# Kernel optimization log

Measured on AMD Instinct MI355X. Metric: run time of the kernel, lower is better.

## Reference

```python
import jax, jax.numpy as jnp
import numpy as np

BS, S, D_IN, D_EMB = 256, 256, 512, 1024
RATIO = 0.3
BN_EPS = 1e-5
VOCAB = 49408


def setup_inputs() -> dict:
    key = jax.random.key(0)
    ks = jax.random.split(key, 12)
    features = jax.random.normal(ks[0], (BS, S, D_IN), dtype=jnp.float32)
    # variable-length token sequences: nonzero ids up to length, 0-padded
    lengths = jax.random.randint(ks[1], (BS,), 3, S + 1)
    tok = jax.random.randint(ks[2], (BS, S), 1, VOCAB)
    text = jnp.where(jnp.arange(S)[None, :] < lengths[:, None], tok, 0).astype(jnp.int32)
    atten = jax.random.normal(ks[3], (BS, S, S), dtype=jnp.float32)
    sc = 0.02
    H = D_EMB // 2  # 512, MLP hidden
    params = {
        "lin_w": jax.random.normal(ks[4], (D_IN, D_EMB), dtype=jnp.float32) * sc,
        "lin_b": jnp.zeros((D_EMB,), dtype=jnp.float32),
        "w1": jax.random.normal(ks[5], (D_IN, H), dtype=jnp.float32) * sc,
        "b1": jnp.zeros((H,), dtype=jnp.float32),
        "g1": jnp.ones((H,), dtype=jnp.float32),
        "be1": jnp.zeros((H,), dtype=jnp.float32),
        "w2": jax.random.normal(ks[6], (H, D_EMB), dtype=jnp.float32) * sc,
        "b2": jnp.zeros((D_EMB,), dtype=jnp.float32),
        "g2": jnp.ones((D_EMB,), dtype=jnp.float32),
        "be2": jnp.zeros((D_EMB,), dtype=jnp.float32),
    }
    return {"features": features, "text": text, "atten": atten, **params}


def _bn_train(x, g, b):
    # BatchNorm1d in train mode: biased batch stats over rows
    m = x.mean(axis=0)
    v = x.var(axis=0)
    return (x - m) * jax.lax.rsqrt(v + BN_EPS) * g + b


def reference(features, text, atten, lin_w, lin_b, w1, b1, g1, be1, w2, b2, g2, be2):
    bs, seq_len = atten.shape[0], atten.shape[1]
    mask = (text != 0).astype(jnp.float32)          # (bs, S)
    token_lens = mask.sum(axis=1)                   # (bs,)
    k = max(1, int((seq_len - 2) * RATIO))          # static
    eos_pos = jnp.clip(token_lens - 1, 0, seq_len - 1).astype(jnp.int32)
    bidx = jnp.arange(bs)
    # scatter writes into atten (faithful to torch in-place updates)
    atten = atten.at[:, :, 0].set(-1.0)
    atten = atten.at[bidx, :, eos_pos].set(-1.0)
    atten = atten.at[bidx, eos_pos, :].set(-1.0)
    atten_sel = atten[bidx, eos_pos, :] * mask      # (bs, S)
    _, topk_idx = jax.lax.top_k(atten_sel, k)       # (bs, k)
    feats_k = jnp.take_along_axis(features, topk_idx[:, :, None], axis=1)  # (bs,k,D_in)
    norm = jnp.maximum(jnp.linalg.norm(feats_k, axis=-1, keepdims=True), 1e-6)
    feats_k = feats_k / norm
    # linear branch
    cap_emb = jnp.einsum("bkd,de->bke", feats_k, lin_w) + lin_b
    # MLP branch: Linear -> BN -> ReLU -> Linear (last layer no BN/ReLU)
    x = feats_k.reshape(bs * k, -1)
    h = jax.nn.relu(_bn_train(x @ w1 + b1, g1, be1))
    o = (h @ w2 + b2).reshape(bs, k, -1)
    fused = o + cap_emb                             # (bs,k,D_emb)
    # maxk_pool1d_var with k=1: max over first pool_lens[i] positions
    pool_lens = jnp.clip(token_lens - 2, 1, k).astype(jnp.int32)
    valid = jnp.arange(k)[None, :] < pool_lens[:, None]  # (bs,k)
    out = jnp.max(jnp.where(valid[:, :, None], fused, -jnp.inf), axis=1)
    return out.astype(jnp.float32)
```

## Files before the change

### kernel.cpp

```cpp
#include <hip/hip_runtime.h>
#include <hip/hip_bf16.h>

typedef __bf16 bf16;
typedef __bf16 bf16x4 __attribute__((ext_vector_type(4)));
typedef __bf16 bf16x8 __attribute__((ext_vector_type(8)));
typedef float  f32x4  __attribute__((ext_vector_type(4)));

#define BSZ   256
#define SEQ   256
#define DIN   512
#define DEMB  1024
#define KSEL  76
#define MROWS (BSZ * KSEL)
#define MT256 (MROWS / 256)
#define PART76 (MT256 * 512)
#define NRED  19

__device__ __forceinline__ void gload16(const void* g, void* l) {
  __builtin_amdgcn_global_load_lds((const __attribute__((address_space(1))) void*)g,
                                   (__attribute__((address_space(3))) void*)l, 16, 0, 0);
}

__device__ __forceinline__ unsigned enc(float v) {
  unsigned u = __float_as_uint(v);
  return (u & 0x80000000u) ? ~u : (u | 0x80000000u);
}
__device__ __forceinline__ float dec(unsigned k) {
  return (k & 0x80000000u) ? __uint_as_float(k ^ 0x80000000u) : __uint_as_float(~k);
}

__global__ void k_setup(const int* __restrict__ text, int* __restrict__ topk,
                        int* __restrict__ plen, uint4* __restrict__ keys4,
                        const float* __restrict__ w1, bf16* __restrict__ w1t,
                        const float* __restrict__ lin_w, const float* __restrict__ w2,
                        bf16* __restrict__ b2t,
                        const float* __restrict__ lin_b, const float* __restrict__ b2,
                        float* __restrict__ bias2) {
  int blk = blockIdx.x, tid = threadIdx.x;
  if (blk < 256) {
    int b = blk;
    keys4[b * 256 + tid] = make_uint4(0u, 0u, 0u, 0u);
    __shared__ int red[256];
    red[tid] = (text[b * SEQ + tid] != 0) ? 1 : 0;
    __syncthreads();
    for (int s = 128; s > 0; s >>= 1) {
      if (tid < s) red[tid] += red[tid + s];
      __syncthreads();
    }
    int len = red[0];
    int z = SEQ - len;
    if (tid < KSEL) topk[b * KSEL + tid] = (tid < z) ? (len + tid) : (tid - z);
    if (tid == 0) {
      int p = len - 2;
      plen[b] = p < 1 ? 1 : (p > KSEL ? KSEL : p);
    }
  } else if (blk < 1536) {
    const float* W;
    bf16* Wt;
    int N, ldo, bx, by;
    if (blk < 512)       { int t = blk - 256;  W = w1;    Wt = w1t;       N = 512;  ldo = 512;  bx = t & 15; by = t >> 4; }
    else if (blk < 1024) { int t = blk - 512;  W = lin_w; Wt = b2t;       N = 1024; ldo = 1024; bx = t & 31; by = t >> 5; }
    else                 { int t = blk - 1024; W = w2;    Wt = b2t + 512; N = 1024; ldo = 1024; bx = t & 31; by = t >> 5; }
    __shared__ float tile[32][33];
    int tx = tid & 31, ty = tid >> 5;
    int n = bx * 32 + tx, k0 = by * 32;
#pragma unroll
    for (int r = 0; r < 32; r += 8)
      tile[ty + r][tx] = W[(size_t)(k0 + ty + r) * N + n];
    __syncthreads();
#pragma unroll
    for (int r = 0; r < 32; r += 8)
      Wt[(size_t)(bx * 32 + ty + r) * ldo + k0 + tx] = (bf16)tile[tx][ty + r];
  } else {
    int i = (blk - 1536) * 256 + tid;
    bias2[i] = lin_b[i] + b2[i];
  }
}

__global__ void k_gather(const float* __restrict__ feats, const int* __restrict__ topk,
                         bf16* __restrict__ A2) {
  int r = blockIdx.x;
  int b = r / KSEL;
  int src = topk[r];
  const float4* row = (const float4*)(feats + ((size_t)b * SEQ + src) * DIN);
  int t = threadIdx.x;
  float4 v = row[t];
  float ss = v.x * v.x + v.y * v.y + v.z * v.z + v.w * v.w;
#pragma unroll
  for (int o = 32; o > 0; o >>= 1) ss += __shfl_down(ss, o);
  __shared__ float wsum[2];
  if ((t & 63) == 0) wsum[t >> 6] = ss;
  __syncthreads();
  float total = wsum[0] + wsum[1];
  float inv = 1.0f / fmaxf(sqrtf(total), 1e-6f);
  bf16x4 o4;
  o4.x = (bf16)(v.x * inv);
  o4.y = (bf16)(v.y * inv);
  o4.z = (bf16)(v.z * inv);
  o4.w = (bf16)(v.w * inv);
  ((bf16x4*)A2)[(size_t)r * 256 + t] = o4;
}

template<int EPI>
__global__ __launch_bounds__(512, 2)
void k_gemm(const bf16* __restrict__ A, int lda, const bf16* __restrict__ Bt, int ldb,
            const float* __restrict__ bias, bf16* __restrict__ Cb, int ldc, int Kext,
            int nbx, float* __restrict__ part, const int* __restrict__ plen,
            unsigned* __restrict__ keys) {
  __shared__ __align__(16) bf16 As[3][256 * 64];
  __shared__ __align__(16) bf16 Bs[3][128 * 64];
  const int q = gridDim.x >> 3;
  const int lid = blockIdx.x;
  const int wg = (lid & 7) * q + (lid >> 3);
  const int bx = wg % nbx, by = wg / nbx;
  const int m0 = by * 256, n0 = bx * 128;
  const int tid = threadIdx.x, wid = tid >> 6, lane = tid & 63;
  const int wm = wid >> 1, wn = wid & 1;
  const int srow = lane >> 3;
  const int scol = ((lane & 7) ^ srow) * 8;
  const bf16* Ag = A + (size_t)(m0 + wid * 16 + srow) * lda + scol;
  const bf16* Bg = Bt + (size_t)(n0 + wid * 16 + srow) * ldb + scol;
  const int nT = Kext >> 6;
  f32x4 acc[4][4] = {};
  const int fr = lane & 15, fg = lane >> 4;

  auto stageA = [&](int t, int buf) {
    const int kt = t << 6;
#pragma unroll
    for (int c = 0; c < 2; ++c) {
      gload16(Ag + (size_t)(c * 8) * lda + kt, &As[buf][(wid * 16 + c * 8) * 64]);
      gload16(Ag + (size_t)(128 + c * 8) * lda + kt, &As[buf][(128 + wid * 16 + c * 8) * 64]);
    }
  };
  auto stageB = [&](int t, int buf) {
    const int kt = t << 6;
#pragma unroll
    for (int c = 0; c < 2; ++c)
      gload16(Bg + (size_t)(c * 8) * ldb + kt, &Bs[buf][(wid * 16 + c * 8) * 64]);
  };

  stageA(0, 0); stageB(0, 0);
  stageA(1, 1); stageB(1, 1);
  asm volatile("s_waitcnt vmcnt(6)" ::: "memory");
  __builtin_amdgcn_s_barrier();
  __builtin_amdgcn_sched_barrier(0);

  int pb = 0, ps = 2;
  for (int t = 0; t < nT; ++t) {
    bf16x8 a0[4], b0[4], a1[4], b1[4];
#pragma unroll
    for (int i = 0; i < 4; ++i)
      a0[i] = *(const bf16x8*)&As[pb][(wm * 64 + i * 16 + fr) * 64 + (fg ^ (fr & 7)) * 8];
#pragma unroll
    for (int j = 0; j < 4; ++j)
      b0[j] = *(const bf16x8*)&Bs[pb][(wn * 64 + j * 16 + fr) * 64 + (fg ^ (fr & 7)) * 8];
    __builtin_amdgcn_sched_barrier(0);
    if (t + 2 < nT) stageA(t + 2, ps);
#pragma unroll
    for (int i = 0; i < 4; ++i)
      a1[i] = *(const bf16x8*)&As[pb][(wm * 64 + i * 16 + fr) * 64 + ((4 | fg) ^ (fr & 7)) * 8];
#pragma unroll
    for (int j = 0; j < 4; ++j)
      b1[j] = *(const bf16x8*)&Bs[pb][(wn * 64 + j * 16 + fr) * 64 + ((4 | fg) ^ (fr & 7)) * 8];
    if (t + 2 < nT) stageB(t + 2, ps);
    asm volatile("s_waitcnt lgkmcnt(8)" ::: "memory");
    __builtin_amdgcn_sched_barrier(0);
    __builtin_amdgcn_s_setprio(1);
#pragma unroll
    for (int i = 0; i < 4; ++i)
#pragma unroll
      for (int j = 0; j < 4; ++j)
        acc[i][j] = __builtin_amdgcn_mfma_f32_16x16x32_bf16(a0[i], b0[j], acc[i][j], 0, 0, 0);
    __builtin_amdgcn_s_setprio(0);
    asm volatile("s_waitcnt lgkmcnt(0)" ::: "memory");
    __builtin_amdgcn_sched_barrier(0);
    __builtin_amdgcn_s_setprio(1);
#pragma unroll
    for (int i = 0; i < 4; ++i)
#pragma unroll
      for (int j = 0; j < 4; ++j)
        acc[i][j] = __builtin_amdgcn_mfma_f32_16x16x32_bf16(a1[i], b1[j], acc[i][j], 0, 0, 0);
    __builtin_amdgcn_s_setprio(0);
    if (t + 2 < nT) {
      asm volatile("s_waitcnt vmcnt(6)" ::: "memory");
    } else {
      asm volatile("s_waitcnt vmcnt(0)" ::: "memory");
    }
    __builtin_amdgcn_s_barrier();
    __builtin_amdgcn_sched_barrier(0);
    pb = (pb == 2) ? 0 : pb + 1;
    ps = (ps == 2) ? 0 : ps + 1;
  }

  float bv[4];
#pragma unroll
  for (int j = 0; j < 4; ++j) bv[j] = bias[n0 + wn * 64 + j * 16 + fr];

  if (EPI == 1) {
    float s[4] = {0, 0, 0, 0}, qq_[4] = {0, 0, 0, 0};
#pragma unroll
    for (int i = 0; i < 4; ++i)
#pragma unroll
      for (int v = 0; v < 4; ++v) {
        int r = m0 + wm * 64 + i * 16 + fg * 4 + v;
        bf16* crow = Cb + (size_t)r * ldc + n0 + wn * 64 + fr;
#pragma unroll
        for (int j = 0; j < 4; ++j) {
          float val = acc[i][j][v] + bv[j];
          crow[j * 16] = (bf16)val;
          s[j] += val;
          qq_[j] += val * val;
        }
      }
#pragma unroll
    for (int j = 0; j < 4; ++j) {
      s[j] += __shfl_down(s[j], 32); s[j] += __shfl_down(s[j], 16);
      qq_[j] += __shfl_down(qq_[j], 32); qq_[j] += __shfl_down(qq_[j], 16);
    }
    __syncthreads();
    float* red = (float*)&As[0][0];
    if (lane < 16) {
#pragma unroll
      for (int j = 0; j < 4; ++j) {
        red[(wid * 4 + j) * 16 + lane] = s[j];
        red[512 + (wid * 4 + j) * 16 + lane] = qq_[j];
      }
    }
    __syncthreads();
    if (tid < 128) {
      int c = tid;
      int wnsel = c >> 6, jj = (c >> 4) & 3, ff = c & 15;
      float ss = 0, qs = 0;
#pragma unroll
      for (int wmi = 0; wmi < 4; ++wmi) {
        ss += red[((wmi * 2 + wnsel) * 4 + jj) * 16 + ff];
        qs += red[512 + ((wmi * 2 + wnsel) * 4 + jj) * 16 + ff];
      }
      part[by * 512 + n0 + c] = ss;
      part[PART76 + by * 512 + n0 + c] = qs;
    }
  } else {
    const float NEG = -__builtin_huge_valf();
    int cur_b = -1, pl = 0;
    bool any = false;
    float cm[4] = {NEG, NEG, NEG, NEG};
#pragma unroll
    for (int i = 0; i < 4; ++i)
#pragma unroll
      for (int v = 0; v < 4; ++v) {
        int gr = m0 + wm * 64 + i * 16 + fg * 4 + v;
        int b = gr / KSEL;
        if (b != cur_b) {
          if (any) {
#pragma unroll
            for (int j = 0; j < 4; ++j)
              atomicMax(&keys[(size_t)cur_b * DEMB + n0 + wn * 64 + j * 16 + fr], enc(cm[j]));
          }
          cur_b = b;
          pl = plen[b];
          any = false;
#pragma unroll
          for (int j = 0; j < 4; ++j) cm[j] = NEG;
        }
        if (gr - b * KSEL < pl) {
          any = true;
#pragma unroll
          for (int j = 0; j < 4; ++j) cm[j] = fmaxf(cm[j], acc[i][j][v] + bv[j]);
        }
      }
    if (any) {
#pragma unroll
      for (int j = 0; j < 4; ++j)
        atomicMax(&keys[(size_t)cur_b * DEMB + n0 + wn * 64 + j * 16 + fr], enc(cm[j]));
    }
  }
}

__global__ void k_bnredA(const float* __restrict__ part, float* __restrict__ part2) {
  int i = blockIdx.x, t = threadIdx.x;
  float s0 = 0, s1 = 0, q0 = 0, q1 = 0;
  for (int j = 0; j < 4; ++j) {
    const float* p = part + (size_t)(i * 4 + j) * 512 + t * 2;
    float2 v = *(const float2*)p;
    float2 u = *(const float2*)(p + PART76);
    s0 += v.x; s1 += v.y; q0 += u.x; q1 += u.y;
  }
  part2[i * 512 + t * 2] = s0;
  part2[i * 512 + t * 2 + 1] = s1;
  part2[NRED * 512 + i * 512 + t * 2] = q0;
  part2[NRED * 512 + i * 512 + t * 2 + 1] = q1;
}

__global__ void k_bnstats(const float* __restrict__ part2, const float* __restrict__ g1,
                          const float* __restrict__ be1, float* __restrict__ bns) {
  int c = threadIdx.x;
  float s = 0, q = 0;
  for (int i = 0; i < NRED; ++i) {
    s += part2[i * 512 + c];
    q += part2[NRED * 512 + i * 512 + c];
  }
  const float invn = 1.0f / (float)MROWS;
  float mean = s * invn;
  float var = q * invn - mean * mean;
  float sc = rsqrtf(var + 1e-5f) * g1[c];
  bns[c] = sc;
  bns[512 + c] = be1[c] - mean * sc;
}

__global__ void k_bnapply(bf16x8* __restrict__ A2v, const float* __restrict__ bns) {
  size_t idx = (size_t)blockIdx.x * 256 + threadIdx.x;
  size_t row = idx >> 6;
  int c = (int)(idx & 63);
  bf16x8* p = A2v + row * 128 + 64 + c;
  bf16x8 v = *p;
  int c8 = c * 8;
  const float4 s0 = *(const float4*)(bns + c8);
  const float4 s1 = *(const float4*)(bns + c8 + 4);
  const float4 h0 = *(const float4*)(bns + 512 + c8);
  const float4 h1 = *(const float4*)(bns + 512 + c8 + 4);
  bf16x8 o;
  o[0] = (bf16)fmaxf(fmaf((float)v[0], s0.x, h0.x), 0.0f);
  o[1] = (bf16)fmaxf(fmaf((float)v[1], s0.y, h0.y), 0.0f);
  o[2] = (bf16)fmaxf(fmaf((float)v[2], s0.z, h0.z), 0.0f);
  o[3] = (bf16)fmaxf(fmaf((float)v[3], s0.w, h0.w), 0.0f);
  o[4] = (bf16)fmaxf(fmaf((float)v[4], s1.x, h1.x), 0.0f);
  o[5] = (bf16)fmaxf(fmaf((float)v[5], s1.y, h1.y), 0.0f);
  o[6] = (bf16)fmaxf(fmaf((float)v[6], s1.z, h1.z), 0.0f);
  o[7] = (bf16)fmaxf(fmaf((float)v[7], s1.w, h1.w), 0.0f);
  *p = o;
}

__global__ void k_decode(const unsigned* __restrict__ keys, float* __restrict__ out) {
  int i = blockIdx.x * 256 + threadIdx.x;
  out[i] = dec(keys[i]);
}

extern "C" void kernel_launch(void* const* d_in, const int* in_sizes, int n_in,
                              void* d_out, int out_size, void* d_ws, size_t ws_size,
                              hipStream_t stream) {
  const float* features = (const float*)d_in[0];
  const int*   text     = (const int*)d_in[1];
  const float* lin_w    = (const float*)d_in[3];
  const float* lin_b    = (const float*)d_in[4];
  const float* w1       = (const float*)d_in[5];
  const float* b1       = (const float*)d_in[6];
  const float* g1       = (const float*)d_in[7];
  const float* be1      = (const float*)d_in[8];
  const float* w2       = (const float*)d_in[9];
  const float* b2       = (const float*)d_in[10];
  float* out = (float*)d_out;
  char* ws = (char*)d_ws;

  int*      topk  = (int*)(ws + 0);
  int*      plen  = (int*)(ws + 77824);
  float*    bns   = (float*)(ws + 78848);
  float*    bias2 = (float*)(ws + 82944);
  float*    part  = (float*)(ws + 87040);
  float*    part2 = (float*)(ws + 398336);
  bf16*     w1t   = (bf16*)(ws + 476160);
  bf16*     b2t   = (bf16*)(ws + 1000448);
  bf16*     A2    = (bf16*)(ws + 3097600);
  unsigned* keys  = (unsigned*)(ws + 42943488);

  k_setup<<<1540, 256, 0, stream>>>(text, topk, plen, (uint4*)keys,
                                    w1, w1t, lin_w, w2, b2t, lin_b, b2, bias2);
  k_gather<<<MROWS, 128, 0, stream>>>(features, topk, A2);
  k_gemm<1><<<MT256 * 4, 512, 0, stream>>>(A2, 1024, w1t, 512, b1, A2 + 512, 1024,
                                           512, 4, part, nullptr, nullptr);
  k_bnredA<<<NRED, 256, 0, stream>>>(part, part2);
  k_bnstats<<<1, 512, 0, stream>>>(part2, g1, be1, bns);
  k_bnapply<<<4864, 256, 0, stream>>>((bf16x8*)A2, bns);
  k_gemm<2><<<MT256 * 8, 512, 0, stream>>>(A2, 1024, b2t, 1024, bias2, nullptr, 0,
                                           1024, 8, nullptr, plen, keys);
  k_decode<<<BSZ * DEMB / 256, 256, 0, stream>>>(keys, out);
}
```

Measured before the change: 130.7 us.

## Restructure GEMM to 4 waves with 128x64 warp tiles and K=32 stages

The GEMM block drops from 8 waves to 4, and each wave now computes a 128x64 output tile (8x4 MFMA fragments) instead of 64x64. The K step per stage goes from 64 to 32, which halves LDS use per buffer, and the XOR swizzle is changed to match the 32-wide rows. The two-half interleaving of LDS reads with MFMAs is replaced by a single load-wait-compute phase. The goal is more register-level reuse per LDS fragment and higher occupancy from the smaller LDS footprint, at the cost of more accumulator registers, more barriers per K, and less overlap inside each wave.

```diff
diff --git a/kernel.cpp b/kernel.cpp
--- a/kernel.cpp
+++ b/kernel.cpp
@@ -102,94 +102,67 @@
 }
 
 template<int EPI>
-__global__ __launch_bounds__(512, 2)
+__global__ __launch_bounds__(256, 2)
 void k_gemm(const bf16* __restrict__ A, int lda, const bf16* __restrict__ Bt, int ldb,
             const float* __restrict__ bias, bf16* __restrict__ Cb, int ldc, int Kext,
             int nbx, float* __restrict__ part, const int* __restrict__ plen,
             unsigned* __restrict__ keys) {
-  __shared__ __align__(16) bf16 As[3][256 * 64];
-  __shared__ __align__(16) bf16 Bs[3][128 * 64];
+  __shared__ __align__(16) bf16 As[3][256 * 32];
+  __shared__ __align__(16) bf16 Bs[3][128 * 32];
   const int q = gridDim.x >> 3;
-  const int lid = blockIdx.x;
-  const int wg = (lid & 7) * q + (lid >> 3);
+  const int wg = (blockIdx.x & 7) * q + (blockIdx.x >> 3);
   const int bx = wg % nbx, by = wg / nbx;
   const int m0 = by * 256, n0 = bx * 128;
-  const int tid = threadIdx.x, wid = tid >> 6, lane = tid & 63;
-  const int wm = wid >> 1, wn = wid & 1;
-  const int srow = lane >> 3;
-  const int scol = ((lane & 7) ^ srow) * 8;
-  const bf16* Ag = A + (size_t)(m0 + wid * 16 + srow) * lda + scol;
-  const bf16* Bg = Bt + (size_t)(n0 + wid * 16 + srow) * ldb + scol;
-  const int nT = Kext >> 6;
-  f32x4 acc[4][4] = {};
+  const int tid = threadIdx.x, w = tid >> 6, lane = tid & 63;
+  const int wm = w >> 1, wn = w & 1;
+  const int srow = lane >> 2;
+  const int scol = (((lane & 3) ^ ((lane >> 2) & 3) ^ ((lane >> 4) & 3))) * 8;
+  const bf16* Ag = A + (size_t)(m0 + w * 64 + srow) * lda + scol;
+  const bf16* Bg = Bt + (size_t)(n0 + w * 32 + srow) * ldb + scol;
+  const int nT = Kext >> 5;
+  f32x4 acc[8][4] = {};
   const int fr = lane & 15, fg = lane >> 4;
-
-  auto stageA = [&](int t, int buf) {
-    const int kt = t << 6;
-#pragma unroll
-    for (int c = 0; c < 2; ++c) {
-      gload16(Ag + (size_t)(c * 8) * lda + kt, &As[buf][(wid * 16 + c * 8) * 64]);
-      gload16(Ag + (size_t)(128 + c * 8) * lda + kt, &As[buf][(128 + wid * 16 + c * 8) * 64]);
-    }
+  const int sl = (fg ^ (fr & 3) ^ ((fr >> 2) & 3)) * 8;
+
+  auto stage = [&](int t, int buf) {
+    const int kt = t << 5;
+#pragma unroll
+    for (int c = 0; c < 4; ++c)
+      gload16(Ag + (size_t)(c * 16) * lda + kt, &As[buf][(w * 64 + c * 16) * 32]);
+#pragma unroll
+    for (int c = 0; c < 2; ++c)
+      gload16(Bg + (size_t)(c * 16) * ldb + kt, &Bs[buf][(w * 32 + c * 16) * 32]);
   };
-  auto stageB = [&](int t, int buf) {
-    const int kt = t << 6;
-#pragma unroll
-    for (int c = 0; c < 2; ++c)
-      gload16(Bg + (size_t)(c * 8) * ldb + kt, &Bs[buf][(wid * 16 + c * 8) * 64]);
-  };
-
-  stageA(0, 0); stageB(0, 0);
-  stageA(1, 1); stageB(1, 1);
+
+  stage(0, 0);
+  stage(1, 1);
   asm volatile("s_waitcnt vmcnt(6)" ::: "memory");
   __builtin_amdgcn_s_barrier();
   __builtin_amdgcn_sched_barrier(0);
 
-  int pb = 0, ps = 2;
   for (int t = 0; t < nT; ++t) {
-    bf16x8 a0[4], b0[4], a1[4], b1[4];
-#pragma unroll
-    for (int i = 0; i < 4; ++i)
-      a0[i] = *(const bf16x8*)&As[pb][(wm * 64 + i * 16 + fr) * 64 + (fg ^ (fr & 7)) * 8];
+    const int pb = t % 3;
+    if (t + 2 < nT) stage(t + 2, (t + 2) % 3);
+    bf16x8 Af[8], Bf[4];
+#pragma unroll
+    for (int i = 0; i < 8; ++i)
+      Af[i] = *(const bf16x8*)&As[pb][(wm * 128 + i * 16 + fr) * 32 + sl];
 #pragma unroll
     for (int j = 0; j < 4; ++j)
-      b0[j] = *(const bf16x8*)&Bs[pb][(wn * 64 + j * 16 + fr) * 64 + (fg ^ (fr & 7)) * 8];
-    __builtin_amdgcn_sched_barrier(0);
-    if (t + 2 < nT) stageA(t + 2, ps);
-#pragma unroll
-    for (int i = 0; i < 4; ++i)
-      a1[i] = *(const bf16x8*)&As[pb][(wm * 64 + i * 16 + fr) * 64 + ((4 | fg) ^ (fr & 7)) * 8];
-#pragma unroll
-    for (int j = 0; j < 4; ++j)
-      b1[j] = *(const bf16x8*)&Bs[pb][(wn * 64 + j * 16 + fr) * 64 + ((4 | fg) ^ (fr & 7)) * 8];
-    if (t + 2 < nT) stageB(t + 2, ps);
-    asm volatile("s_waitcnt lgkmcnt(8)" ::: "memory");
-    __builtin_amdgcn_sched_barrier(0);
-    __builtin_amdgcn_s_setprio(1);
-#pragma unroll
-    for (int i = 0; i < 4; ++i)
-#pragma unroll
-      for (int j = 0; j < 4; ++j)
-        acc[i][j] = __builtin_amdgcn_mfma_f32_16x16x32_bf16(a0[i], b0[j], acc[i][j], 0, 0, 0);
-    __builtin_amdgcn_s_setprio(0);
+      Bf[j] = *(const bf16x8*)&Bs[pb][(wn * 64 + j * 16 + fr) * 32 + sl];
     asm volatile("s_waitcnt lgkmcnt(0)" ::: "memory");
     __builtin_amdgcn_sched_barrier(0);
     __builtin_amdgcn_s_setprio(1);
 #pragma unroll
-    for (int i = 0; i < 4; ++i)
+    for (int i = 0; i < 8; ++i)
 #pragma unroll
       for (int j = 0; j < 4; ++j)
-        acc[i][j] = __builtin_amdgcn_mfma_f32_16x16x32_bf16(a1[i], b1[j], acc[i][j], 0, 0, 0);
+        acc[i][j] = __builtin_amdgcn_mfma_f32_16x16x32_bf16(Af[i], Bf[j], acc[i][j], 0, 0, 0);
     __builtin_amdgcn_s_setprio(0);
-    if (t + 2 < nT) {
-      asm volatile("s_waitcnt vmcnt(6)" ::: "memory");
-    } else {
-      asm volatile("s_waitcnt vmcnt(0)" ::: "memory");
-    }
+    if (t + 2 < nT) asm volatile("s_waitcnt vmcnt(6)" ::: "memory");
+    else            asm volatile("s_waitcnt vmcnt(0)" ::: "memory");
     __builtin_amdgcn_s_barrier();
     __builtin_amdgcn_sched_barrier(0);
-    pb = (pb == 2) ? 0 : pb + 1;
-    ps = (ps == 2) ? 0 : ps + 1;
   }
 
   float bv[4];
@@ -199,10 +172,10 @@
   if (EPI == 1) {
     float s[4] = {0, 0, 0, 0}, qq_[4] = {0, 0, 0, 0};
 #pragma unroll
-    for (int i = 0; i < 4; ++i)
+    for (int i = 0; i < 8; ++i)
 #pragma unroll
       for (int v = 0; v < 4; ++v) {
-        int r = m0 + wm * 64 + i * 16 + fg * 4 + v;
+        int r = m0 + wm * 128 + i * 16 + fg * 4 + v;
         bf16* crow = Cb + (size_t)r * ldc + n0 + wn * 64 + fr;
 #pragma unroll
         for (int j = 0; j < 4; ++j) {
@@ -222,20 +195,17 @@
     if (lane < 16) {
 #pragma unroll
       for (int j = 0; j < 4; ++j) {
-        red[(wid * 4 + j) * 16 + lane] = s[j];
-        red[512 + (wid * 4 + j) * 16 + lane] = qq_[j];
+        red[(w * 4 + j) * 16 + lane] = s[j];
+        red[512 + (w * 4 + j) * 16 + lane] = qq_[j];
       }
     }
     __syncthreads();
     if (tid < 128) {
       int c = tid;
-      int wnsel = c >> 6, jj = (c >> 4) & 3, ff = c & 15;
-      float ss = 0, qs = 0;
-#pragma unroll
-      for (int wmi = 0; wmi < 4; ++wmi) {
-        ss += red[((wmi * 2 + wnsel) * 4 + jj) * 16 + ff];
-        qs += red[512 + ((wmi * 2 + wnsel) * 4 + jj) * 16 + ff];
-      }
+      int wsel = c >> 6, jj = (c >> 4) & 3, ff = c & 15;
+      float ss = red[(wsel * 4 + jj) * 16 + ff] + red[((wsel + 2) * 4 + jj) * 16 + ff];
+      float qs = red[512 + (wsel * 4 + jj) * 16 + ff] +
+                 red[512 + ((wsel + 2) * 4 + jj) * 16 + ff];
       part[by * 512 + n0 + c] = ss;
       part[PART76 + by * 512 + n0 + c] = qs;
     }
@@ -245,10 +215,10 @@
     bool any = false;
     float cm[4] = {NEG, NEG, NEG, NEG};
 #pragma unroll
-    for (int i = 0; i < 4; ++i)
+    for (int i = 0; i < 8; ++i)
 #pragma unroll
       for (int v = 0; v < 4; ++v) {
-        int gr = m0 + wm * 64 + i * 16 + fg * 4 + v;
+        int gr = m0 + wm * 128 + i * 16 + fg * 4 + v;
         int b = gr / KSEL;
         if (b != cur_b) {
           if (any) {
@@ -365,12 +335,12 @@
   k_setup<<<1540, 256, 0, stream>>>(text, topk, plen, (uint4*)keys,
                                     w1, w1t, lin_w, w2, b2t, lin_b, b2, bias2);
   k_gather<<<MROWS, 128, 0, stream>>>(features, topk, A2);
-  k_gemm<1><<<MT256 * 4, 512, 0, stream>>>(A2, 1024, w1t, 512, b1, A2 + 512, 1024,
+  k_gemm<1><<<MT256 * 4, 256, 0, stream>>>(A2, 1024, w1t, 512, b1, A2 + 512, 1024,
                                            512, 4, part, nullptr, nullptr);
   k_bnredA<<<NRED, 256, 0, stream>>>(part, part2);
   k_bnstats<<<1, 512, 0, stream>>>(part2, g1, be1, bns);
   k_bnapply<<<4864, 256, 0, stream>>>((bf16x8*)A2, bns);
-  k_gemm<2><<<MT256 * 8, 512, 0, stream>>>(A2, 1024, b2t, 1024, bias2, nullptr, 0,
+  k_gemm<2><<<MT256 * 8, 256, 0, stream>>>(A2, 1024, b2t, 1024, bias2, nullptr, 0,
                                            1024, 8, nullptr, plen, keys);
   k_decode<<<BSZ * DEMB / 256, 256, 0, stream>>>(keys, out);
 }
```

After: 136.0 us. +4.1%, slower.
